# Optimization experiments

Measured on AMD Instinct MI355X. Metric: run time of the kernel, lower is better.

The kernel has to match this reference:

```python
import jax, jax.numpy as jnp
import numpy as np

B = 8192
E = 8
H = 128
NUM_CLASSES = 3
SIM_THRESHOLD = 0.8
EFF_THRESHOLD = 0.1
TARGET_TEMP = 1.0
W_LB, W_EFF, W_CONS, W_ENT, W_TEMP = 0.1, 0.05, 0.1, 0.01, 0.01


def setup_inputs() -> dict:
    key = jax.random.key(0)
    k1, k2, k3, k4 = jax.random.split(key, 4)
    logits = jax.random.normal(k1, (B, NUM_CLASSES), dtype=jnp.float32)
    targets = jax.random.randint(k2, (B,), 0, NUM_CLASSES, dtype=jnp.int64)
    raw = jax.random.uniform(k3, (B, E), dtype=jnp.float32)
    routing_probs = raw / raw.sum(axis=-1, keepdims=True)  # rows sum to 1
    input_embeddings = jax.random.uniform(k4, (B, H), dtype=jnp.float32)
    temperature = jnp.ones((1,), dtype=jnp.float32)
    return {
        "logits": logits,
        "targets": targets,
        "routing_probs": routing_probs,
        "input_embeddings": input_embeddings,
        "temperature": temperature,
    }


def _dynamo_loss(logits, routing_probs, input_embeddings, temperature, targets):
    # --- task loss: cross entropy (sentiment) ---
    logp_cls = jax.nn.log_softmax(logits, axis=-1)
    task_loss = -jnp.take_along_axis(logp_cls, targets[:, None], axis=-1).mean()

    # --- load balance: var(mean usage) / (1/E)^2 (torch.var unbiased) ---
    expert_usage = routing_probs.mean(axis=0)  # [E]
    lb_loss = W_LB * jnp.var(expert_usage, ddof=1) * (E ** 2)

    # --- efficiency: sum of probs below threshold, averaged over batch ---
    small = jnp.where(routing_probs < EFF_THRESHOLD, routing_probs, 0.0)
    eff_loss = W_EFF * small.sum(axis=-1).mean()

    # --- consistency: masked pairwise KL over similar samples ---
    nrm = input_embeddings / jnp.linalg.norm(input_embeddings, axis=-1, keepdims=True)
    sim = nrm @ nrm.T  # [B, B]
    mask = (sim > SIM_THRESHOLD) & ~jnp.eye(B, dtype=bool)
    logp = jax.nn.log_softmax(routing_probs, axis=-1)  # [B, E]
    p = jnp.exp(logp)
    a = jnp.sum(p * logp, axis=-1)  # [B], sum_e p_j log p_j
    # KL(i,j) = sum_e p_j (log p_j - log p_i) = a[j] - logp[i] . p[j]
    kl = a[None, :] - logp @ p.T  # [B, B]
    num_pairs = mask.sum()
    kl_sum = jnp.sum(jnp.where(mask, kl, 0.0))
    cons_loss = W_CONS * jnp.where(num_pairs > 0, kl_sum / jnp.maximum(num_pairs, 1), 0.0)

    # --- entropy regularization (maximize entropy of routing_probs-as-probs) ---
    eps = 1e-8
    entropy = -jnp.sum(routing_probs * jnp.log(routing_probs + eps), axis=-1)
    ent_loss = W_ENT * (-entropy.mean())

    # --- temperature regularization ---
    temp_loss = W_TEMP * jnp.mean((temperature - TARGET_TEMP) ** 2)

    return task_loss + lb_loss + eff_loss + cons_loss + ent_loss + temp_loss


def reference(logits, targets, routing_probs, input_embeddings, temperature):
    return _dynamo_loss(logits, routing_probs, input_embeddings, temperature, targets)
```

## Files before the change

### kernel.cpp

```cpp
#include <hip/hip_runtime.h>
#include <stdint.h>

#define B_SZ 8192
#define LOG8 2.0794415416798357f
#define NTILE 2080

typedef __attribute__((ext_vector_type(8))) short short8;
typedef __attribute__((ext_vector_type(4))) float floatx4;

typedef __attribute__((address_space(1))) const uint4 guint4;
typedef __attribute__((address_space(3))) uint4 luint4;

__device__ inline void async_cp16(const uint4* g, uint4* l) {
    __builtin_amdgcn_global_load_lds((guint4*)g, (luint4*)l, 16, 0, 0);
}

__device__ inline unsigned short f2bf(float f) {
    unsigned int u = __float_as_uint(f);
    u = (u + 0x7FFFu + ((u >> 16) & 1u)) >> 16;
    return (unsigned short)u;
}
__device__ inline float bf2f(unsigned short s) {
    return __uint_as_float(((unsigned int)s) << 16);
}
__device__ inline float wredf(float x) {
#pragma unroll
    for (int o = 32; o; o >>= 1) x += __shfl_down(x, o);
    return x;
}
__device__ inline int wredi(int x) {
#pragma unroll
    for (int o = 32; o; o >>= 1) x += __shfl_down(x, o);
    return x;
}


__global__ __launch_bounds__(512) void prep_all(
    const float* __restrict__ logits,
    const int* __restrict__ targets,
    const float* __restrict__ routing,
    const float* __restrict__ emb,
    unsigned short* __restrict__ nrm,
    unsigned short* __restrict__ nlq,
    unsigned short* __restrict__ pb,
    float* __restrict__ aprime,
    float* __restrict__ prepslot) {
    const int bid = blockIdx.x;
    const int lane = threadIdx.x & 63;
    const int wave = threadIdx.x >> 6;

#pragma unroll
    for (int iter = 0; iter < 4; ++iter) {
        int row = (((iter << 8) + bid) << 3) + wave;
        const float2* e2 = (const float2*)(emb + (size_t)row * 128);
        float2 vv = e2[lane];
        float ss = vv.x * vv.x + vv.y * vv.y;
        ss = wredf(ss);
        ss = __shfl(ss, 0);
        float inv = rsqrtf(ss);
        ushort2 o;
        o.x = f2bf(vv.x * inv);
        o.y = f2bf(vv.y * inv);
        ((ushort2*)(nrm + (size_t)row * 128))[lane] = o;
    }

    if (wave != 0) return;

    float task = 0.f, eff = 0.f, ent = 0.f;
    float v[8] = {0.f, 0.f, 0.f, 0.f, 0.f, 0.f, 0.f, 0.f};

    if (lane < 32) {
        int row = (bid << 5) + lane;

        const float4* r4 = (const float4*)(routing + (size_t)row * 8);
        float4 va = r4[0], vb = r4[1];
        v[0] = va.x; v[1] = va.y; v[2] = va.z; v[3] = va.w;
        v[4] = vb.x; v[5] = vb.y; v[6] = vb.z; v[7] = vb.w;

        float mx = v[0];
#pragma unroll
        for (int e = 1; e < 8; ++e) mx = fmaxf(mx, v[e]);
        float ex[8], s = 0.f;
#pragma unroll
        for (int e = 0; e < 8; ++e) { ex[e] = expf(v[e] - mx); s += ex[e]; }
        float ls = logf(s);
        float inv_s = 1.f / s;

        union { unsigned short u[8]; uint4 q; } lu, pu;
        float ap = 0.f;
#pragma unroll
        for (int e = 0; e < 8; ++e) {
            unsigned short pe = f2bf(ex[e] * inv_s);
            unsigned short le = f2bf(v[e] - mx - ls + LOG8);
            pu.u[e] = pe;
            lu.u[e] = le ^ 0x8000;
            ap += bf2f(pe) * bf2f(le);
        }
        ((uint4*)nlq)[row] = lu.q;
        ((uint4*)pb)[row] = pu.q;
        aprime[row] = ap;

#pragma unroll
        for (int e = 0; e < 8; ++e) {
            if (v[e] < 0.1f) eff += v[e];
            ent += v[e] * logf(v[e] + 1e-8f);
        }

        const float* lg = logits + (size_t)row * 3;
        float a0 = lg[0], a1 = lg[1], a2 = lg[2];
        float mm = fmaxf(a0, fmaxf(a1, a2));
        float lse = mm + logf(expf(a0 - mm) + expf(a1 - mm) + expf(a2 - mm));
        int tg = targets[row];
        float tv = (tg == 0) ? a0 : ((tg == 1) ? a1 : a2);
        task = lse - tv;
    }

    task = wredf(task);
    eff = wredf(eff);
    ent = wredf(ent);
    float cs[8];
#pragma unroll
    for (int e = 0; e < 8; ++e) cs[e] = wredf(v[e]);

    if (lane == 0) {
        float* ps = prepslot + bid * 11;
        ps[0] = task;
        ps[1] = eff;
        ps[2] = ent;
#pragma unroll
        for (int e = 0; e < 8; ++e) ps[3 + e] = cs[e];
    }
}

__global__ __launch_bounds__(512, 6) void tile_sym(
    const unsigned short* __restrict__ nrm,
    const unsigned short* __restrict__ nlq,
    const unsigned short* __restrict__ pb,
    const float* __restrict__ aprime,
    float* __restrict__ klslot,
    unsigned int* __restrict__ cntslot) {
    __shared__ uint4 sh[2048];

    const int t = threadIdx.x;
    const int L = blockIdx.x;
    const int wave = t >> 6, lane = t & 63;

    int bi = (int)((129.0f - sqrtf((float)(16641 - 8 * L))) * 0.5f);
    int T = bi * 64 - ((bi * (bi - 1)) >> 1);
    while (L < T) { --bi; T = bi * 64 - ((bi * (bi - 1)) >> 1); }
    while (L >= T + (64 - bi)) { T += 64 - bi; ++bi; }
    const int bj = bi + (L - T);
    const bool diag = (bi == bj);
    const int iBase = bi << 7, jBase = bj << 7;

    const uint4* n4 = (const uint4*)nrm;
    const int s0 = t & 7, r0 = t >> 3;
    const int s1 = (t + 512) & 7, r1 = (t + 512) >> 3;
    const int g0 = s0 ^ (r0 & 7), g1 = s1 ^ (r1 & 7);

    async_cp16(&n4[((size_t)(iBase + r0) << 4) + g0], sh + (wave << 6));
    async_cp16(&n4[((size_t)(iBase + r1) << 4) + g1], sh + 512 + (wave << 6));
    async_cp16(&n4[((size_t)(jBase + r0) << 4) + g0], sh + 1024 + (wave << 6));
    async_cp16(&n4[((size_t)(jBase + r1) << 4) + g1], sh + 1536 + (wave << 6));

    const int wr = wave >> 2, wc = wave & 3;
    const int m = lane & 15, q = lane >> 4;

    floatx4 simacc[4][2];
#pragma unroll
    for (int a = 0; a < 4; ++a)
#pragma unroll
        for (int b = 0; b < 2; ++b) simacc[a][b] = (floatx4){0.f, 0.f, 0.f, 0.f};

    const int m7 = m & 7;
    const int raOff = (wr << 6) << 3;
    const int rbOff = (wc << 5) << 3;

    __syncthreads();

#pragma unroll
    for (int ks = 0; ks < 2; ++ks) {
        const int sg = ((ks << 2) + q) ^ m7;
        short8 af[4], bfr[2];
#pragma unroll
        for (int a = 0; a < 4; ++a)
            af[a] = *(const short8*)(sh + raOff + (((a << 4) + m) << 3) + sg);
#pragma unroll
        for (int b = 0; b < 2; ++b)
            bfr[b] = *(const short8*)(sh + 1024 + rbOff + (((b << 4) + m) << 3) + sg);
#pragma unroll
        for (int a = 0; a < 4; ++a)
#pragma unroll
            for (int b = 0; b < 2; ++b)
                simacc[a][b] = __builtin_amdgcn_mfma_f32_16x16x32_bf16(
                    af[a], bfr[b], simacc[a][b], 0, 0, 0);
    }

    __syncthreads();

    async_cp16(&n4[((size_t)(iBase + r0) << 4) + 8 + g0], sh + (wave << 6));
    async_cp16(&n4[((size_t)(iBase + r1) << 4) + 8 + g1], sh + 512 + (wave << 6));
    async_cp16(&n4[((size_t)(jBase + r0) << 4) + 8 + g0], sh + 1024 + (wave << 6));
    async_cp16(&n4[((size_t)(jBase + r1) << 4) + 8 + g1], sh + 1536 + (wave << 6));

    __syncthreads();

#pragma unroll
    for (int ks = 0; ks < 2; ++ks) {
        const int sg = ((ks << 2) + q) ^ m7;
        short8 af[4], bfr[2];
#pragma unroll
        for (int a = 0; a < 4; ++a)
            af[a] = *(const short8*)(sh + raOff + (((a << 4) + m) << 3) + sg);
#pragma unroll
        for (int b = 0; b < 2; ++b)
            bfr[b] = *(const short8*)(sh + 1024 + rbOff + (((b << 4) + m) << 3) + sg);
#pragma unroll
        for (int a = 0; a < 4; ++a)
#pragma unroll
            for (int b = 0; b < 2; ++b)
                simacc[a][b] = __builtin_amdgcn_mfma_f32_16x16x32_bf16(
                    af[a], bfr[b], simacc[a][b], 0, 0, 0);
    }

    const short8 zero8 = (short8){0, 0, 0, 0, 0, 0, 0, 0};
    short8 crA[4], crB[2];
#pragma unroll
    for (int a = 0; a < 4; ++a) {
        int ri = iBase + (wr << 6) + (a << 4) + m;
        short8 v = zero8;
        if (q == 0) v = *(const short8*)&nlq[(size_t)ri << 3];
        else if (q == 1) { if (!diag) v = *(const short8*)&pb[(size_t)ri << 3]; }
        else if (q == 2) {
            v[1] = (short)0x3F80;
            if (!diag) v[0] = (short)f2bf(aprime[ri]);
        }
        crA[a] = v;
    }
#pragma unroll
    for (int b = 0; b < 2; ++b) {
        int cj = jBase + (wc << 5) + (b << 4) + m;
        short8 v = zero8;
        if (q == 0) v = *(const short8*)&pb[(size_t)cj << 3];
        else if (q == 1) v = *(const short8*)&nlq[(size_t)cj << 3];
        else if (q == 2) {
            v[0] = (short)0x3F80;
            v[1] = (short)f2bf(aprime[cj]);
        }
        crB[b] = v;
    }

    float klLocal = 0.f;
    int cntLocal = 0;
#pragma unroll
    for (int a = 0; a < 4; ++a) {
        const int gRow0 = iBase + (wr << 6) + (a << 4) + (q << 2);
#pragma unroll
        for (int b = 0; b < 2; ++b) {
            const int gCol = jBase + (wc << 5) + (b << 4) + m;
            floatx4 cr = __builtin_amdgcn_mfma_f32_16x16x32_bf16(
                crA[a], crB[b], (floatx4){0.f, 0.f, 0.f, 0.f}, 0, 0, 0);
            if (diag) {
#pragma unroll
                for (int r = 0; r < 4; ++r) {
                    if ((simacc[a][b][r] > 0.8f) && (gRow0 + r != gCol)) {
                        klLocal += cr[r];
                        cntLocal += 1;
                    }
                }
            } else {
#pragma unroll
                for (int r = 0; r < 4; ++r) {
                    if (simacc[a][b][r] > 0.8f) {
                        klLocal += cr[r];
                        cntLocal += 2;
                    }
                }
            }
        }
    }

    klLocal = wredf(klLocal);
    cntLocal = wredi(cntLocal);

    __syncthreads();
    float* redk = (float*)sh;
    int* redc = (int*)(redk + 8);
    if (lane == 0) { redk[wave] = klLocal; redc[wave] = cntLocal; }
    __syncthreads();

    if (t == 0) {
        float k = 0.f;
        int c = 0;
#pragma unroll
        for (int w = 0; w < 8; ++w) { k += redk[w]; c += redc[w]; }
        klslot[L] = k;
        cntslot[L] = (unsigned int)c;
    }
}

__global__ void finalize_k(const float* __restrict__ klslot,
                           const unsigned int* __restrict__ cntslot,
                           const float* __restrict__ prepslot,
                           const float* __restrict__ temp,
                           float* __restrict__ out) {
    __shared__ float sk[4];
    __shared__ int sc[4];
    __shared__ float sp[4][11];
    const int t = threadIdx.x, lane = t & 63, wave = t >> 6;

    float k = 0.f;
    int c = 0;
    for (int i = t; i < NTILE; i += 256) { k += klslot[i]; c += (int)cntslot[i]; }
    k = wredf(k);
    c = wredi(c);
    if (lane == 0) { sk[wave] = k; sc[wave] = c; }

    float sv[11];
    const float* ps = prepslot + t * 11;
#pragma unroll
    for (int j = 0; j < 11; ++j) sv[j] = ps[j];
#pragma unroll
    for (int j = 0; j < 11; ++j) sv[j] = wredf(sv[j]);
    if (lane == 0) {
#pragma unroll
        for (int j = 0; j < 11; ++j) sp[wave][j] = sv[j];
    }
    __syncthreads();

    if (t == 0) {
        float K = sk[0] + sk[1] + sk[2] + sk[3];
        int C = sc[0] + sc[1] + sc[2] + sc[3];
        float st[11];
#pragma unroll
        for (int j = 0; j < 11; ++j)
            st[j] = sp[0][j] + sp[1][j] + sp[2][j] + sp[3][j];
        const float invB = 1.f / (float)B_SZ;
        float task = st[0] * invB;
        float eff = 0.05f * st[1] * invB;
        float entl = 0.01f * st[2] * invB;
        float cons = 0.1f * (C > 0 ? K / (float)C : 0.f);
        float u[8], mean = 0.f;
#pragma unroll
        for (int e = 0; e < 8; ++e) { u[e] = st[3 + e] * invB; mean += u[e]; }
        mean *= 0.125f;
        float var = 0.f;
#pragma unroll
        for (int e = 0; e < 8; ++e) { float d = u[e] - mean; var += d * d; }
        var *= (1.f / 7.f);
        float lb = 0.1f * var * 64.f;
        float tt = temp[0] - 1.f;
        out[0] = task + lb + eff + cons + entl + 0.01f * tt * tt;
    }
}

extern "C" void kernel_launch(void* const* d_in, const int* in_sizes, int n_in,
                              void* d_out, int out_size, void* d_ws, size_t ws_size,
                              hipStream_t stream) {
    const float* logits = (const float*)d_in[0];
    const int* targets = (const int*)d_in[1];
    const float* routing = (const float*)d_in[2];
    const float* emb = (const float*)d_in[3];
    const float* temp = (const float*)d_in[4];

    char* ws = (char*)d_ws;
    unsigned short* nrm = (unsigned short*)ws;
    unsigned short* nlq = (unsigned short*)(ws + 2097152);
    unsigned short* pb = (unsigned short*)(ws + 2228224);
    float* aprime = (float*)(ws + 2359296);
    float* klslot = (float*)(ws + 2392064);
    unsigned int* cntslot = (unsigned int*)(ws + 2400384);
    float* prepslot = (float*)(ws + 2408704);

    prep_all<<<256, 512, 0, stream>>>(logits, targets, routing, emb,
                                      nrm, nlq, pb, aprime, prepslot);
    tile_sym<<<NTILE, 512, 0, stream>>>(nrm, nlq, pb, aprime, klslot, cntslot);
    finalize_k<<<1, 256, 0, stream>>>(klslot, cntslot, prepslot, temp,
                                      (float*)d_out);
}
```

Baseline: 97.75 us.

## Load MFMA operands directly from global memory instead of staging through LDS

Result: slower. 141.3 us (+44.5%).

```diff
diff --git a/kernel.cpp b/kernel.cpp
--- a/kernel.cpp
+++ b/kernel.cpp
@@ -7,13 +7,6 @@
 
 typedef __attribute__((ext_vector_type(8))) short short8;
 typedef __attribute__((ext_vector_type(4))) float floatx4;
-
-typedef __attribute__((address_space(1))) const uint4 guint4;
-typedef __attribute__((address_space(3))) uint4 luint4;
-
-__device__ inline void async_cp16(const uint4* g, uint4* l) {
-    __builtin_amdgcn_global_load_lds((guint4*)g, (luint4*)l, 16, 0, 0);
-}
 
 __device__ inline unsigned short f2bf(float f) {
     unsigned int u = __float_as_uint(f);
@@ -139,7 +132,8 @@
     const float* __restrict__ aprime,
     float* __restrict__ klslot,
     unsigned int* __restrict__ cntslot) {
-    __shared__ uint4 sh[2048];
+    __shared__ float redk[8];
+    __shared__ int redc[8];
 
     const int t = threadIdx.x;
     const int L = blockIdx.x;
@@ -153,68 +147,28 @@
     const bool diag = (bi == bj);
     const int iBase = bi << 7, jBase = bj << 7;
 
-    const uint4* n4 = (const uint4*)nrm;
-    const int s0 = t & 7, r0 = t >> 3;
-    const int s1 = (t + 512) & 7, r1 = (t + 512) >> 3;
-    const int g0 = s0 ^ (r0 & 7), g1 = s1 ^ (r1 & 7);
-
-    async_cp16(&n4[((size_t)(iBase + r0) << 4) + g0], sh + (wave << 6));
-    async_cp16(&n4[((size_t)(iBase + r1) << 4) + g1], sh + 512 + (wave << 6));
-    async_cp16(&n4[((size_t)(jBase + r0) << 4) + g0], sh + 1024 + (wave << 6));
-    async_cp16(&n4[((size_t)(jBase + r1) << 4) + g1], sh + 1536 + (wave << 6));
-
     const int wr = wave >> 2, wc = wave & 3;
     const int m = lane & 15, q = lane >> 4;
 
+    const unsigned short* Abase = nrm + ((size_t)(iBase + (wr << 6)) << 7);
+    const unsigned short* Bbase = nrm + ((size_t)(jBase + (wc << 5)) << 7);
+
     floatx4 simacc[4][2];
 #pragma unroll
     for (int a = 0; a < 4; ++a)
 #pragma unroll
         for (int b = 0; b < 2; ++b) simacc[a][b] = (floatx4){0.f, 0.f, 0.f, 0.f};
 
-    const int m7 = m & 7;
-    const int raOff = (wr << 6) << 3;
-    const int rbOff = (wc << 5) << 3;
-
-    __syncthreads();
-
-#pragma unroll
-    for (int ks = 0; ks < 2; ++ks) {
-        const int sg = ((ks << 2) + q) ^ m7;
+#pragma unroll
+    for (int ks = 0; ks < 4; ++ks) {
+        const int ko = ((ks << 2) + q) << 3;
         short8 af[4], bfr[2];
 #pragma unroll
         for (int a = 0; a < 4; ++a)
-            af[a] = *(const short8*)(sh + raOff + (((a << 4) + m) << 3) + sg);
+            af[a] = *(const short8*)(Abase + ((((a << 4) + m) << 7) + ko));
 #pragma unroll
         for (int b = 0; b < 2; ++b)
-            bfr[b] = *(const short8*)(sh + 1024 + rbOff + (((b << 4) + m) << 3) + sg);
-#pragma unroll
-        for (int a = 0; a < 4; ++a)
-#pragma unroll
-            for (int b = 0; b < 2; ++b)
-                simacc[a][b] = __builtin_amdgcn_mfma_f32_16x16x32_bf16(
-                    af[a], bfr[b], simacc[a][b], 0, 0, 0);
-    }
-
-    __syncthreads();
-
-    async_cp16(&n4[((size_t)(iBase + r0) << 4) + 8 + g0], sh + (wave << 6));
-    async_cp16(&n4[((size_t)(iBase + r1) << 4) + 8 + g1], sh + 512 + (wave << 6));
-    async_cp16(&n4[((size_t)(jBase + r0) << 4) + 8 + g0], sh + 1024 + (wave << 6));
-    async_cp16(&n4[((size_t)(jBase + r1) << 4) + 8 + g1], sh + 1536 + (wave << 6));
-
-    __syncthreads();
-
-#pragma unroll
-    for (int ks = 0; ks < 2; ++ks) {
-        const int sg = ((ks << 2) + q) ^ m7;
-        short8 af[4], bfr[2];
-#pragma unroll
-        for (int a = 0; a < 4; ++a)
-            af[a] = *(const short8*)(sh + raOff + (((a << 4) + m) << 3) + sg);
-#pragma unroll
-        for (int b = 0; b < 2; ++b)
-            bfr[b] = *(const short8*)(sh + 1024 + rbOff + (((b << 4) + m) << 3) + sg);
+            bfr[b] = *(const short8*)(Bbase + ((((b << 4) + m) << 7) + ko));
 #pragma unroll
         for (int a = 0; a < 4; ++a)
 #pragma unroll
@@ -283,9 +237,6 @@
     klLocal = wredf(klLocal);
     cntLocal = wredi(cntLocal);
 
-    __syncthreads();
-    float* redk = (float*)sh;
-    int* redc = (int*)(redk + 8);
     if (lane == 0) { redk[wave] = klLocal; redc[wave] = cntLocal; }
     __syncthreads();
 
```
